# Optimization experiments

Hardware: AMD Instinct MI355X
Metric: run time of the kernel (lower is better)

## Reference

```python
import jax, jax.numpy as jnp
import numpy as np

DIM = 2048
N_HEADS = 16
N_KV_HEADS = 4
HEAD_DIM = DIM // N_HEADS  # 128
ROPE_BASE = 10000.0
QK_GAIN_INIT = 1.0
RMS_EPS = 1.1920928955078125e-07  # torch F.rms_norm default eps = finfo(fp32).eps


def _rms_norm(x):
    # normalize over last dim, no learned gain
    var = jnp.mean(jnp.square(x), axis=-1, keepdims=True)
    return x * jax.lax.rsqrt(var + RMS_EPS)


def _rope_cos_sin(seq_len, dtype):
    half = HEAD_DIM // 2
    inv_freq = 1.0 / (ROPE_BASE ** (jnp.arange(0, HEAD_DIM, 2, dtype=jnp.float32) / HEAD_DIM))
    t = jnp.arange(seq_len, dtype=jnp.float32)
    freqs = jnp.outer(t, inv_freq)  # [S, half]
    return jnp.cos(freqs).astype(dtype), jnp.sin(freqs).astype(dtype)


def _apply_rotary(x, cos, sin):
    # x: [B, H, S, D]; cos/sin: [S, D//2] broadcast over B,H
    half = x.shape[-1] // 2
    x1, x2 = x[..., :half], x[..., half:]
    return jnp.concatenate((x1 * cos + x2 * sin, x1 * (-sin) + x2 * cos), axis=-1)


def setup_inputs() -> dict:
    key = jax.random.key(0)
    ks = jax.random.split(key, 6)
    B, S = 2, 2048
    kv_dim = N_KV_HEADS * HEAD_DIM
    x = jax.random.normal(ks[0], (B, S, DIM), dtype=jnp.float32)
    Wq = jax.random.normal(ks[1], (DIM, DIM), dtype=jnp.float32) * (DIM ** -0.5)
    Wk = jax.random.normal(ks[2], (kv_dim, DIM), dtype=jnp.float32) * (DIM ** -0.5)
    Wv = jax.random.normal(ks[3], (kv_dim, DIM), dtype=jnp.float32) * (DIM ** -0.5)
    Wproj = jax.random.normal(ks[4], (DIM, DIM), dtype=jnp.float32) * (DIM ** -0.5)
    q_gain = jnp.full((N_HEADS,), QK_GAIN_INIT, dtype=jnp.float32)
    return {"x": x, "Wq": Wq, "Wk": Wk, "Wv": Wv, "Wproj": Wproj, "q_gain": q_gain}


def reference(x, Wq, Wk, Wv, Wproj, q_gain):
    B, S, D = x.shape
    G = N_HEADS // N_KV_HEADS  # GQA group size
    # QKV projections (CastedLinear, no bias)
    q = (x @ Wq.T).reshape(B, S, N_HEADS, HEAD_DIM).transpose(0, 2, 1, 3)      # [B,H,S,d]
    k = (x @ Wk.T).reshape(B, S, N_KV_HEADS, HEAD_DIM).transpose(0, 2, 1, 3)   # [B,Hkv,S,d]
    v = (x @ Wv.T).reshape(B, S, N_KV_HEADS, HEAD_DIM).transpose(0, 2, 1, 3)
    # QK RMS-norm
    q = _rms_norm(q)
    k = _rms_norm(k)
    # RoPE (scaling='none' -> attention_factor = 1.0)
    cos, sin = _rope_cos_sin(S, q.dtype)
    q = _apply_rotary(q, cos, sin)
    k = _apply_rotary(k, cos, sin)
    # per-head query gain * attention_factor (=1.0)
    q = q * q_gain.astype(q.dtype)[None, :, None, None]
    # causal GQA SDPA: group queries by kv head, no k/v materialized repeats
    qg = q.reshape(B, N_KV_HEADS, G, S, HEAD_DIM)
    scale = 1.0 / jnp.sqrt(jnp.asarray(HEAD_DIM, dtype=q.dtype))
    scores = jnp.einsum('bkgqd,bkld->bkgql', qg, k) * scale  # [B,Hkv,G,S,S]
    causal = jnp.tril(jnp.ones((S, S), dtype=bool))
    scores = jnp.where(causal, scores, jnp.asarray(-jnp.inf, dtype=scores.dtype))
    attn = jax.nn.softmax(scores, axis=-1)
    y = jnp.einsum('bkgql,bkld->bkgqd', attn, v)              # [B,Hkv,G,S,d]
    y = y.reshape(B, N_HEADS, S, HEAD_DIM).transpose(0, 2, 1, 3).reshape(B, S, D)
    return y @ Wproj.T
```

## Files before the change

### kernel.cpp

```cpp
#include <hip/hip_runtime.h>
#include <hip/hip_bf16.h>

#define DIM 2048
#define NH 16
#define NKV 4
#define HD 128
#define S_LEN 2048
#define BATCH 2
#define QKV_N 3072
#define NEGBIG -1.0e30f

typedef __attribute__((ext_vector_type(8))) short bf16x8;
typedef __attribute__((ext_vector_type(4))) float f32x4;
typedef unsigned short ushort_t;

#define GLOAD_LDS16(gp, lp)                                                       \
    __builtin_amdgcn_global_load_lds(                                             \
        (const __attribute__((address_space(1))) void*)(gp),                      \
        (__attribute__((address_space(3))) void*)(lp), 16, 0, 0)

static __device__ __forceinline__ ushort_t f2bf(float f) {
    union { float f; unsigned u; } v; v.f = f;
    unsigned r = v.u + 0x7fffu + ((v.u >> 16) & 1u);
    return (ushort_t)(r >> 16);
}
static __device__ __forceinline__ float bf2f(ushort_t u) {
    union { unsigned u; float f; } v; v.u = ((unsigned)u) << 16;
    return v.f;
}
static __device__ __forceinline__ unsigned pk2bf(float a, float b) {
    unsigned r;
    __asm__ volatile("v_cvt_pk_bf16_f32 %0, %1, %2" : "=v"(r) : "v"(a), "v"(b));
    return r;
}

__global__ __launch_bounds__(256) void cvt_in(const float* __restrict__ x,
                                              const float* __restrict__ Wq,
                                              const float* __restrict__ Wk,
                                              const float* __restrict__ Wv,
                                              const float* __restrict__ Wp,
                                              ushort_t* __restrict__ xb,
                                              ushort_t* __restrict__ Wqkvb,
                                              ushort_t* __restrict__ Wpb) {
    int i = (blockIdx.x * 256 + threadIdx.x) * 4;
    const float* src;
    ushort_t* dst;
    int soff, doff;
    if (i < 8388608) {
        src = x; dst = xb; soff = i; doff = i;
    } else if (i < 14680064) {
        int j = i - 8388608;
        dst = Wqkvb; doff = j;
        if (j < 4194304) { src = Wq; soff = j; }
        else if (j < 5242880) { src = Wk; soff = j - 4194304; }
        else { src = Wv; soff = j - 5242880; }
    } else {
        int j = i - 14680064;
        src = Wp; dst = Wpb; soff = j; doff = j;
    }
    float4 v = *(const float4*)&src[soff];
    uint2 o = {pk2bf(v.x, v.y), pk2bf(v.z, v.w)};
    *(uint2*)&dst[doff] = o;
}

#define FENCE() __asm__ __volatile__("" ::: "memory")
#define BARRIER() do { FENCE(); __builtin_amdgcn_s_barrier(); FENCE(); } while (0)
#define WAITVM(n) __asm__ __volatile__("s_waitcnt vmcnt(" #n ")" ::: "memory")
#define WLGKM0() __asm__ __volatile__("s_waitcnt lgkmcnt(0)" ::: "memory")

#define STG(LDSA, GP, rowb) do {                                                  \
    const int r_ = (rowb) + rsub;                                                 \
    GLOAD_LDS16(&(GP)[(size_t)r_ * 2048 + kk0_ + ((csw0 ^ (r_ & 7)) * 8)],        \
                &(LDSA)[(rowb) * 64]);                                            \
} while (0)

#define STAGE_HT(AB, BB, kt, ht) do {                                             \
    const int kt_ = (kt) < 31 ? (kt) : 31;                                        \
    const int kk0_ = kt_ * 64;                                                    \
    if ((ht) == 0)      { STG(BB, Bp, w8);       STG(BB, Bp, 64 + w8);  }         \
    else if ((ht) == 1) { STG(BB, Bp, 128 + w8); STG(BB, Bp, 192 + w8); }         \
    else if ((ht) == 2) { STG(AB, Ap, w8);       STG(AB, Ap, 128 + w8); }         \
    else                { STG(AB, Ap, 64 + w8);  STG(AB, Ap, 192 + w8); }         \
} while (0)

#define DSA(mtb, AS) do {                                                         \
    _Pragma("unroll") for (int dm = 0; dm < 2; dm++)                              \
    _Pragma("unroll") for (int ks = 0; ks < 2; ks++) {                            \
        const int row = wr * 128 + ((mtb) + dm) * 16 + m16;                       \
        af[dm][ks] = *(const bf16x8*)&(AS)[row * 64 +                             \
                                           (((ks * 4 + quad) ^ (row & 7)) * 8)];  \
    }                                                                             \
} while (0)

#define DSB(BS) do {                                                              \
    _Pragma("unroll") for (int nt = 0; nt < 4; nt++)                              \
    _Pragma("unroll") for (int ks = 0; ks < 2; ks++) {                            \
        const int row = wc * 64 + nt * 16 + m16;                                  \
        bfr[nt][ks] = *(const bf16x8*)&(BS)[row * 64 +                            \
                                            (((ks * 4 + quad) ^ (row & 7)) * 8)]; \
    }                                                                             \
} while (0)

#define MMA(mtb) do {                                                             \
    __builtin_amdgcn_s_setprio(1);                                                \
    _Pragma("unroll") for (int ks = 0; ks < 2; ks++)                              \
    _Pragma("unroll") for (int dm = 0; dm < 2; dm++)                              \
    _Pragma("unroll") for (int nt = 0; nt < 4; nt++)                              \
        acc[(mtb) + dm][nt] = __builtin_amdgcn_mfma_f32_16x16x32_bf16(            \
            af[dm][ks], bfr[nt][ks], acc[(mtb) + dm][nt], 0, 0, 0);               \
    __builtin_amdgcn_s_setprio(0);                                                \
} while (0)

template <int EPI>
__global__ __launch_bounds__(512, 2) void gemm256(const ushort_t* __restrict__ A,
                                                  const ushort_t* __restrict__ B,
                                                  float* __restrict__ C,
                                                  ushort_t* __restrict__ qkv,
                                                  ushort_t* __restrict__ vt,
                                                  const float* __restrict__ gain,
                                                  int N) {
    __shared__ __align__(16) ushort_t sh[4][256 * 64];
    const int t = threadIdx.x;
    const int lane = t & 63;
    const int wave = t >> 6;
    const int m16 = lane & 15;
    const int quad = lane >> 4;
    const int wr = wave >> 2;
    const int wc = wave & 3;
    const int nwg = gridDim.x * gridDim.y;
    const int wgid = blockIdx.y * gridDim.x + blockIdx.x;
    const int wg2 = (wgid & 7) * (nwg >> 3) + (wgid >> 3);
    const int bx = wg2 % gridDim.x;
    const int m0 = (wg2 / gridDim.x) * 256;
    const int n0 = bx * 256;
    const int rsub = lane >> 3;
    const int csw0 = lane & 7;
    const int w8 = wave * 8;
    const ushort_t* Ap = A + (size_t)m0 * 2048;
    const ushort_t* Bp = B + (size_t)n0 * 2048;

    f32x4 acc[8][4];
#pragma unroll
    for (int i = 0; i < 8; i++)
#pragma unroll
        for (int j = 0; j < 4; j++) acc[i][j] = (f32x4){0.f, 0.f, 0.f, 0.f};

    STAGE_HT(sh[0], sh[2], 0, 0);
    STAGE_HT(sh[0], sh[2], 0, 1);
    STAGE_HT(sh[0], sh[2], 0, 2);
    STAGE_HT(sh[0], sh[2], 0, 3);
    STAGE_HT(sh[1], sh[3], 1, 0);
    STAGE_HT(sh[1], sh[3], 1, 1);
    STAGE_HT(sh[1], sh[3], 1, 2);
    WAITVM(6);
    BARRIER();

    bf16x8 bfr[4][2];
#pragma unroll 1
    for (int i = 0; i < 16; ++i) {
        const int tb = 2 * i;
        {
            bf16x8 af[2][2];
            DSA(0, sh[0]); DSB(sh[2]);
            STAGE_HT(sh[1], sh[3], tb + 1, 3);
            WLGKM0(); MMA(0); BARRIER();
        }
        {
            bf16x8 af[2][2];
            DSA(2, sh[0]);
            STAGE_HT(sh[0], sh[2], tb + 2, 0);
            WLGKM0(); MMA(2); BARRIER();
        }
        {
            bf16x8 af[2][2];
            DSA(4, sh[0]);
            STAGE_HT(sh[0], sh[2], tb + 2, 1);
            WLGKM0(); MMA(4); BARRIER();
        }
        {
            bf16x8 af[2][2];
            DSA(6, sh[0]);
            STAGE_HT(sh[0], sh[2], tb + 2, 2);
            WAITVM(6);
            WLGKM0(); MMA(6); BARRIER();
        }
        {
            bf16x8 af[2][2];
            DSA(0, sh[1]); DSB(sh[3]);
            STAGE_HT(sh[0], sh[2], tb + 2, 3);
            WLGKM0(); MMA(0); BARRIER();
        }
        {
            bf16x8 af[2][2];
            DSA(2, sh[1]);
            STAGE_HT(sh[1], sh[3], tb + 3, 0);
            WLGKM0(); MMA(2); BARRIER();
        }
        {
            bf16x8 af[2][2];
            DSA(4, sh[1]);
            STAGE_HT(sh[1], sh[3], tb + 3, 1);
            WLGKM0(); MMA(4); BARRIER();
        }
        {
            bf16x8 af[2][2];
            DSA(6, sh[1]);
            STAGE_HT(sh[1], sh[3], tb + 3, 2);
            WAITVM(6);
            WLGKM0(); MMA(6); BARRIER();
        }
    }
    WAITVM(0);
    __syncthreads();

    if constexpr (EPI == 0) {
#pragma unroll
        for (int mt = 0; mt < 8; mt++)
#pragma unroll
            for (int r = 0; r < 4; r++) {
                const int row = m0 + wr * 128 + mt * 16 + quad * 4 + r;
#pragma unroll
                for (int nt = 0; nt < 4; nt++)
                    C[(size_t)row * N + n0 + wc * 64 + nt * 16 + m16] = acc[mt][nt][r];
            }
    } else {
        ushort_t* Cs = &sh[0][0];
#pragma unroll
        for (int mt = 0; mt < 8; mt++)
#pragma unroll
            for (int r = 0; r < 4; r++) {
                const int row = wr * 128 + mt * 16 + quad * 4 + r;
#pragma unroll
                for (int nt = 0; nt < 4; nt++)
                    Cs[row * 256 + wc * 64 + nt * 16 + m16] = f2bf(acc[mt][nt][r]);
            }
        __syncthreads();

        if (bx < 10) {
            const float invf = exp2f(-0.20762050593046f * (float)lane);
            float gg[2];
#pragma unroll
            for (int hh = 0; hh < 2; hh++) gg[hh] = (bx < 8) ? gain[bx * 2 + hh] : 1.0f;
#pragma unroll 2
            for (int i = 0; i < 32; i++) {
                const int row = wave * 32 + i;
                const int m = m0 + row;
                const int s = m & (S_LEN - 1);
                const float fr = (float)s * invf;
                const float c = cosf(fr), sn = sinf(fr);
#pragma unroll
                for (int hh = 0; hh < 2; hh++) {
                    float x1 = bf2f(Cs[row * 256 + hh * 128 + lane]);
                    float x2 = bf2f(Cs[row * 256 + hh * 128 + 64 + lane]);
                    float ss = x1 * x1 + x2 * x2;
#pragma unroll
                    for (int mm = 32; mm >= 1; mm >>= 1) ss += __shfl_xor(ss, mm, 64);
                    const float rms = rsqrtf(ss * (1.0f / 128.0f) + 1.1920928955078125e-07f);
                    x1 *= rms; x2 *= rms;
                    ushort_t* dst = qkv + (size_t)m * QKV_N + bx * 256 + hh * 128;
                    dst[lane] = f2bf((x1 * c + x2 * sn) * gg[hh]);
                    dst[lane + 64] = f2bf((x2 * c - x1 * sn) * gg[hh]);
                }
            }
        } else {
            const int half = t >> 8;
            const int tt = t & 255;
            const int d = tt >> 1;
            const int so = (tt & 1) * 128;
            const int b = m0 >> 11;
            const int s0 = m0 & (S_LEN - 1);
            const int kv = (bx - 10) * 2 + half;
            ushort_t* dst = vt + ((size_t)(b * NKV + kv) * HD + d) * S_LEN + s0 + so;
#pragma unroll
            for (int j0 = 0; j0 < 128; j0 += 8) {
                ushort_t tmp[8];
#pragma unroll
                for (int j = 0; j < 8; j++) tmp[j] = Cs[(so + j0 + j) * 256 + half * 128 + d];
                *(uint4*)&dst[j0] = *(uint4*)tmp;
            }
        }
    }
}

__device__ __constant__ short attn_tab[24][4] = {
    {15, 0, 16, 14}, {15, 16, 32, 15}, {7, 0, 16, -1}, {14, 0, 15, 12},
    {13, 0, 14, 10}, {13, 14, 28, 11}, {6, 0, 14, -1}, {10, 0, 11, 4},
    {12, 0, 13, 8},  {12, 13, 26, 9}, {14, 15, 30, 13}, {11, 0, 12, 6},
    {11, 12, 24, 7}, {5, 0, 12, -1}, {10, 11, 22, 5},  {9, 0, 10, 2},
    {2, 0, 6, -1},   {1, 0, 4, -1},  {0, 0, 2, -1},    {3, 0, 8, -1},
    {8, 0, 9, 0},    {8, 9, 18, 1},  {9, 10, 20, 3},   {4, 0, 10, -1},
};

__global__ __launch_bounds__(256) void attn(const ushort_t* __restrict__ QKV,
                                            const ushort_t* __restrict__ Vt,
                                            ushort_t* __restrict__ Y,
                                            ushort_t* __restrict__ Po,
                                            float* __restrict__ Pl) {
    __shared__ __align__(16) ushort_t Ks[64 * 128];
    __shared__ __align__(16) ushort_t Vs[128 * 64];
    __shared__ __align__(16) ushort_t Ps[4][32 * 72];
    const int lane = threadIdx.x & 63;
    const int wave = threadIdx.x >> 6;
    const int m16 = lane & 15, quad = lane >> 4;
    const int seg = blockIdx.x >> 5;
    const int hb = blockIdx.x & 31;
    const int h = hb & (NH - 1), b = hb >> 4;
    const int kvh = h >> 2;
    const int bx = attn_tab[seg][0];
    const int t0 = attn_tab[seg][1];
    const int t1 = attn_tab[seg][2];
    const int slotl = attn_tab[seg][3];
    const int q0w = bx * 128 + wave * 32;

    const ushort_t* kbase = QKV + (size_t)b * S_LEN * QKV_N + DIM + kvh * HD;
    const ushort_t* vbase = Vt + (size_t)(b * NKV + kvh) * (HD * S_LEN);

    bf16x8 bq[2][4];
#pragma unroll
    for (int g = 0; g < 2; g++)
#pragma unroll
        for (int ks = 0; ks < 4; ks++)
            bq[g][ks] = *(const bf16x8*)&QKV[((size_t)(b * S_LEN + q0w + g * 16 + m16)) * QKV_N +
                                             h * HD + ks * 32 + quad * 8];

    float ls[2] = {0.f, 0.f};
    f32x4 o[2][8];
#pragma unroll
    for (int g = 0; g < 2; g++)
#pragma unroll
        for (int nd = 0; nd < 8; nd++) o[g][nd] = (f32x4){0.f, 0.f, 0.f, 0.f};

    ushort_t* pw = Ps[wave];
    for (int t = t0; t < t1; ++t) {
        const int kv0 = t * 64;
        __syncthreads();
#pragma unroll
        for (int i = 0; i < 4; i++) {
            const int c0 = i * 256 + wave * 64;
            const int ck = c0 + lane;
            const int krow = ck >> 4;
            const int kcol = (ck & 15) ^ (krow & 7);
            GLOAD_LDS16(kbase + (size_t)(kv0 + krow) * QKV_N + kcol * 8, &Ks[c0 * 8]);
            const int vd = ck >> 3;
            const int vcol = (ck & 7) ^ (vd & 7);
            GLOAD_LDS16(vbase + (size_t)vd * S_LEN + kv0 + vcol * 8, &Vs[c0 * 8]);
        }
        __syncthreads();

        f32x4 st[2][4];
#pragma unroll
        for (int g = 0; g < 2; g++)
#pragma unroll
            for (int nt = 0; nt < 4; nt++) st[g][nt] = (f32x4){0.f, 0.f, 0.f, 0.f};
#pragma unroll
        for (int ks = 0; ks < 4; ks++)
#pragma unroll
            for (int nt = 0; nt < 4; nt++) {
                const int row = nt * 16 + m16;
                bf16x8 ak = *(const bf16x8*)&Ks[row * 128 + (((ks * 4 + quad) ^ (row & 7)) * 8)];
#pragma unroll
                for (int g = 0; g < 2; g++)
                    st[g][nt] = __builtin_amdgcn_mfma_f32_16x16x32_bf16(ak, bq[g][ks],
                                                                        st[g][nt], 0, 0, 0);
            }
#pragma unroll
        for (int g = 0; g < 2; g++) {
            const int q0g = q0w + g * 16;
            const int qg = q0g + m16;
            const bool interior = (kv0 + 63 <= q0g);
            float rs = 0.f;
#pragma unroll
            for (int nt = 0; nt < 4; nt++) {
                float p[4];
#pragma unroll
                for (int r = 0; r < 4; r++) {
                    float x = st[g][nt][r] * 0.08838834764831845f;
                    if (!interior) {
                        const int kg = kv0 + nt * 16 + quad * 4 + r;
                        x = (kg > qg) ? NEGBIG : x;
                    }
                    p[r] = __expf(x);
                }
                rs += (p[0] + p[1]) + (p[2] + p[3]);
                uint2 pk = {pk2bf(p[0], p[1]), pk2bf(p[2], p[3])};
                *(uint2*)&pw[(g * 16 + m16) * 72 + nt * 16 + quad * 4] = pk;
            }
            ls[g] += rs;
        }
        __asm__ __volatile__("s_waitcnt lgkmcnt(0)" ::: "memory");
        bf16x8 bp[2][2];
#pragma unroll
        for (int g = 0; g < 2; g++)
#pragma unroll
            for (int kk = 0; kk < 2; kk++)
                bp[g][kk] = *(const bf16x8*)&pw[(g * 16 + m16) * 72 + kk * 32 + quad * 8];
#pragma unroll
        for (int kk = 0; kk < 2; kk++)
#pragma unroll
            for (int nd = 0; nd < 8; nd++) {
                const int vrow = nd * 16 + m16;
                bf16x8 av = *(const bf16x8*)&Vs[vrow * 64 + (((kk * 4 + quad) ^ (vrow & 7)) * 8)];
#pragma unroll
                for (int g = 0; g < 2; g++)
                    o[g][nd] = __builtin_amdgcn_mfma_f32_16x16x32_bf16(av, bp[g][kk],
                                                                       o[g][nd], 0, 0, 0);
            }
    }
    float l_tot[2];
#pragma unroll
    for (int g = 0; g < 2; g++) {
        float v = ls[g];
        v += __shfl_xor(v, 16, 64);
        v += __shfl_xor(v, 32, 64);
        l_tot[g] = v;
    }
    if (slotl < 0) {
#pragma unroll
        for (int g = 0; g < 2; g++) {
            const float inv = 1.0f / l_tot[g];
            const int qg = q0w + g * 16 + m16;
            ushort_t* yp = Y + ((size_t)(b * S_LEN + qg)) * DIM + h * HD;
#pragma unroll
            for (int nd = 0; nd < 8; nd++) {
                uint2 pk = {pk2bf(o[g][nd][0] * inv, o[g][nd][1] * inv),
                            pk2bf(o[g][nd][2] * inv, o[g][nd][3] * inv)};
                *(uint2*)&yp[nd * 16 + quad * 4] = pk;
            }
        }
    } else if ((slotl & 1) == 0) {
        const int slot = ((b * NH + h) << 4) + slotl;
#pragma unroll
        for (int g = 0; g < 2; g++) {
            const int qg = q0w + g * 16 + m16;
            ushort_t* yp = Y + ((size_t)(b * S_LEN + qg)) * DIM + h * HD;
#pragma unroll
            for (int nd = 0; nd < 8; nd++) {
                uint2 pk = {pk2bf(o[g][nd][0], o[g][nd][1]),
                            pk2bf(o[g][nd][2], o[g][nd][3])};
                *(uint2*)&yp[nd * 16 + quad * 4] = pk;
            }
            if (quad == 0) Pl[slot * 128 + wave * 32 + g * 16 + m16] = l_tot[g];
        }
    } else {
        const int slot = ((b * NH + h) << 4) + slotl;
        ushort_t* po = Po + (size_t)(((b * NH + h) << 3) + (slotl >> 1)) * (128 * 128);
#pragma unroll
        for (int g = 0; g < 2; g++) {
            const int ql = wave * 32 + g * 16 + m16;
#pragma unroll
            for (int nd = 0; nd < 8; nd++) {
                uint2 pk = {pk2bf(o[g][nd][0], o[g][nd][1]),
                            pk2bf(o[g][nd][2], o[g][nd][3])};
                *(uint2*)&po[ql * 128 + nd * 16 + quad * 4] = pk;
            }
            if (quad == 0) Pl[slot * 128 + ql] = l_tot[g];
        }
    }
}

__global__ __launch_bounds__(256) void attn_combine(const ushort_t* __restrict__ Po,
                                                    const float* __restrict__ Pl,
                                                    ushort_t* __restrict__ Y) {
    const int R = blockIdx.x * 2 + (threadIdx.x >> 7);
    const int d = threadIdx.x & 127;
    const int q = R & 127;
    const int bx8 = (R >> 7) & 7;
    const int h = (R >> 10) & 15;
    const int b = R >> 14;
    const int hb16 = ((b * NH + h) << 4);
    const float l0 = Pl[(hb16 + bx8 * 2) * 128 + q];
    const float l1 = Pl[(hb16 + bx8 * 2 + 1) * 128 + q];
    const float inv = 1.0f / (l0 + l1);
    const int qg = (bx8 + 8) * 128 + q;
    ushort_t* yp = Y + ((size_t)(b * S_LEN + qg)) * DIM + h * HD + d;
    const float o0 = bf2f(*yp);
    const float o1 = bf2f(Po[(size_t)(((b * NH + h) << 3) + bx8) * (128 * 128) + q * 128 + d]);
    *yp = f2bf((o0 + o1) * inv);
}

extern "C" void kernel_launch(void* const* d_in, const int* in_sizes, int n_in,
                              void* d_out, int out_size, void* d_ws, size_t ws_size,
                              hipStream_t stream) {
    (void)in_sizes; (void)n_in; (void)out_size; (void)ws_size;
    const float* xf  = (const float*)d_in[0];
    const float* Wqf = (const float*)d_in[1];
    const float* Wkf = (const float*)d_in[2];
    const float* Wvf = (const float*)d_in[3];
    const float* Wpf = (const float*)d_in[4];
    const float* gn  = (const float*)d_in[5];
    float* out = (float*)d_out;

    char* ws = (char*)d_ws;
    ushort_t* xb    = (ushort_t*)(ws);
    ushort_t* qkv   = (ushort_t*)(ws + (16ull << 20));
    ushort_t* vt    = (ushort_t*)(ws + (40ull << 20));
    ushort_t* Wqkvb = (ushort_t*)(ws + (44ull << 20));
    ushort_t* Wpb   = (ushort_t*)(ws + (56ull << 20));
    ushort_t* y     = xb;
    ushort_t* Po    = (ushort_t*)(ws + (44ull << 20));
    float*    Pl    = (float*)(ws + (52ull << 20));

    const int M = BATCH * S_LEN;
    cvt_in<<<dim3(18432), 256, 0, stream>>>(xf, Wqf, Wkf, Wvf, Wpf, xb, Wqkvb, Wpb);
    gemm256<1><<<dim3(QKV_N / 256, M / 256), 512, 0, stream>>>(xb, Wqkvb, nullptr, qkv, vt, gn, 0);
    attn<<<dim3(768, 1, 1), 256, 0, stream>>>(qkv, vt, y, Po, Pl);
    attn_combine<<<dim3(BATCH * NH * 8 * 128 / 2), 256, 0, stream>>>(Po, Pl, y);
    gemm256<0><<<dim3(DIM / 256, M / 256), 512, 0, stream>>>(y, Wpb, out, nullptr, nullptr, nullptr, DIM);
}
```

Before: 305.9 us.

## Use dedicated 128x256-tile pipelined GEMM for output projection

Splits the templated GEMM into a QKV-specific kernel and a new output-projection kernel that uses 128x256 tiles with its own double-buffered LDS staging schedule. The smaller M tile doubles the grid for the 4096x2048x2048 projection from 128 to 256 workgroups, improving occupancy and wave balance across the CUs. The cost is lower arithmetic intensity per tile and more A/B reloads from L2.

```diff
diff --git a/kernel.cpp b/kernel.cpp
--- a/kernel.cpp
+++ b/kernel.cpp
@@ -111,14 +111,11 @@
     __builtin_amdgcn_s_setprio(0);                                                \
 } while (0)
 
-template <int EPI>
-__global__ __launch_bounds__(512, 2) void gemm256(const ushort_t* __restrict__ A,
-                                                  const ushort_t* __restrict__ B,
-                                                  float* __restrict__ C,
-                                                  ushort_t* __restrict__ qkv,
-                                                  ushort_t* __restrict__ vt,
-                                                  const float* __restrict__ gain,
-                                                  int N) {
+__global__ __launch_bounds__(512, 2) void gemm256_qkv(const ushort_t* __restrict__ A,
+                                                      const ushort_t* __restrict__ B,
+                                                      ushort_t* __restrict__ qkv,
+                                                      ushort_t* __restrict__ vt,
+                                                      const float* __restrict__ gain) {
     __shared__ __align__(16) ushort_t sh[4][256 * 64];
     const int t = threadIdx.x;
     const int lane = t & 63;
@@ -159,51 +156,43 @@
 #pragma unroll 1
     for (int i = 0; i < 16; ++i) {
         const int tb = 2 * i;
-        {
-            bf16x8 af[2][2];
+        {   bf16x8 af[2][2];
             DSA(0, sh[0]); DSB(sh[2]);
             STAGE_HT(sh[1], sh[3], tb + 1, 3);
             WLGKM0(); MMA(0); BARRIER();
         }
-        {
-            bf16x8 af[2][2];
+        {   bf16x8 af[2][2];
             DSA(2, sh[0]);
             STAGE_HT(sh[0], sh[2], tb + 2, 0);
             WLGKM0(); MMA(2); BARRIER();
         }
-        {
-            bf16x8 af[2][2];
+        {   bf16x8 af[2][2];
             DSA(4, sh[0]);
             STAGE_HT(sh[0], sh[2], tb + 2, 1);
             WLGKM0(); MMA(4); BARRIER();
         }
-        {
-            bf16x8 af[2][2];
+        {   bf16x8 af[2][2];
             DSA(6, sh[0]);
             STAGE_HT(sh[0], sh[2], tb + 2, 2);
             WAITVM(6);
             WLGKM0(); MMA(6); BARRIER();
         }
-        {
-            bf16x8 af[2][2];
+        {   bf16x8 af[2][2];
             DSA(0, sh[1]); DSB(sh[3]);
             STAGE_HT(sh[0], sh[2], tb + 2, 3);
             WLGKM0(); MMA(0); BARRIER();
         }
-        {
-            bf16x8 af[2][2];
+        {   bf16x8 af[2][2];
             DSA(2, sh[1]);
             STAGE_HT(sh[1], sh[3], tb + 3, 0);
             WLGKM0(); MMA(2); BARRIER();
         }
-        {
-            bf16x8 af[2][2];
+        {   bf16x8 af[2][2];
             DSA(4, sh[1]);
             STAGE_HT(sh[1], sh[3], tb + 3, 1);
             WLGKM0(); MMA(4); BARRIER();
         }
-        {
-            bf16x8 af[2][2];
+        {   bf16x8 af[2][2];
             DSA(6, sh[1]);
             STAGE_HT(sh[1], sh[3], tb + 3, 2);
             WAITVM(6);
@@ -213,73 +202,180 @@
     WAITVM(0);
     __syncthreads();
 
-    if constexpr (EPI == 0) {
-#pragma unroll
-        for (int mt = 0; mt < 8; mt++)
-#pragma unroll
-            for (int r = 0; r < 4; r++) {
-                const int row = m0 + wr * 128 + mt * 16 + quad * 4 + r;
-#pragma unroll
-                for (int nt = 0; nt < 4; nt++)
-                    C[(size_t)row * N + n0 + wc * 64 + nt * 16 + m16] = acc[mt][nt][r];
+    ushort_t* Cs = &sh[0][0];
+#pragma unroll
+    for (int mt = 0; mt < 8; mt++)
+#pragma unroll
+        for (int r = 0; r < 4; r++) {
+            const int row = wr * 128 + mt * 16 + quad * 4 + r;
+#pragma unroll
+            for (int nt = 0; nt < 4; nt++)
+                Cs[row * 256 + wc * 64 + nt * 16 + m16] = f2bf(acc[mt][nt][r]);
+        }
+    __syncthreads();
+
+    if (bx < 10) {
+        const float invf = exp2f(-0.20762050593046f * (float)lane);
+        float gg[2];
+#pragma unroll
+        for (int hh = 0; hh < 2; hh++) gg[hh] = (bx < 8) ? gain[bx * 2 + hh] : 1.0f;
+#pragma unroll 2
+        for (int i = 0; i < 32; i++) {
+            const int row = wave * 32 + i;
+            const int m = m0 + row;
+            const int s = m & (S_LEN - 1);
+            const float fr = (float)s * invf;
+            const float c = cosf(fr), sn = sinf(fr);
+#pragma unroll
+            for (int hh = 0; hh < 2; hh++) {
+                float x1 = bf2f(Cs[row * 256 + hh * 128 + lane]);
+                float x2 = bf2f(Cs[row * 256 + hh * 128 + 64 + lane]);
+                float ss = x1 * x1 + x2 * x2;
+#pragma unroll
+                for (int mm = 32; mm >= 1; mm >>= 1) ss += __shfl_xor(ss, mm, 64);
+                const float rms = rsqrtf(ss * (1.0f / 128.0f) + 1.1920928955078125e-07f);
+                x1 *= rms; x2 *= rms;
+                ushort_t* dst = qkv + (size_t)m * QKV_N + bx * 256 + hh * 128;
+                dst[lane] = f2bf((x1 * c + x2 * sn) * gg[hh]);
+                dst[lane + 64] = f2bf((x2 * c - x1 * sn) * gg[hh]);
             }
+        }
     } else {
-        ushort_t* Cs = &sh[0][0];
-#pragma unroll
-        for (int mt = 0; mt < 8; mt++)
-#pragma unroll
-            for (int r = 0; r < 4; r++) {
-                const int row = wr * 128 + mt * 16 + quad * 4 + r;
-#pragma unroll
-                for (int nt = 0; nt < 4; nt++)
-                    Cs[row * 256 + wc * 64 + nt * 16 + m16] = f2bf(acc[mt][nt][r]);
-            }
-        __syncthreads();
-
-        if (bx < 10) {
-            const float invf = exp2f(-0.20762050593046f * (float)lane);
-            float gg[2];
-#pragma unroll
-            for (int hh = 0; hh < 2; hh++) gg[hh] = (bx < 8) ? gain[bx * 2 + hh] : 1.0f;
-#pragma unroll 2
-            for (int i = 0; i < 32; i++) {
-                const int row = wave * 32 + i;
-                const int m = m0 + row;
-                const int s = m & (S_LEN - 1);
-                const float fr = (float)s * invf;
-                const float c = cosf(fr), sn = sinf(fr);
-#pragma unroll
-                for (int hh = 0; hh < 2; hh++) {
-                    float x1 = bf2f(Cs[row * 256 + hh * 128 + lane]);
-                    float x2 = bf2f(Cs[row * 256 + hh * 128 + 64 + lane]);
-                    float ss = x1 * x1 + x2 * x2;
-#pragma unroll
-                    for (int mm = 32; mm >= 1; mm >>= 1) ss += __shfl_xor(ss, mm, 64);
-                    const float rms = rsqrtf(ss * (1.0f / 128.0f) + 1.1920928955078125e-07f);
-                    x1 *= rms; x2 *= rms;
-                    ushort_t* dst = qkv + (size_t)m * QKV_N + bx * 256 + hh * 128;
-                    dst[lane] = f2bf((x1 * c + x2 * sn) * gg[hh]);
-                    dst[lane + 64] = f2bf((x2 * c - x1 * sn) * gg[hh]);
-                }
-            }
-        } else {
-            const int half = t >> 8;
-            const int tt = t & 255;
-            const int d = tt >> 1;
-            const int so = (tt & 1) * 128;
-            const int b = m0 >> 11;
-            const int s0 = m0 & (S_LEN - 1);
-            const int kv = (bx - 10) * 2 + half;
-            ushort_t* dst = vt + ((size_t)(b * NKV + kv) * HD + d) * S_LEN + s0 + so;
-#pragma unroll
-            for (int j0 = 0; j0 < 128; j0 += 8) {
-                ushort_t tmp[8];
-#pragma unroll
-                for (int j = 0; j < 8; j++) tmp[j] = Cs[(so + j0 + j) * 256 + half * 128 + d];
-                *(uint4*)&dst[j0] = *(uint4*)tmp;
-            }
+        const int half = t >> 8;
+        const int tt = t & 255;
+        const int d = tt >> 1;
+        const int so = (tt & 1) * 128;
+        const int b = m0 >> 11;
+        const int s0 = m0 & (S_LEN - 1);
+        const int kv = (bx - 10) * 2 + half;
+        ushort_t* dst = vt + ((size_t)(b * NKV + kv) * HD + d) * S_LEN + s0 + so;
+#pragma unroll
+        for (int j0 = 0; j0 < 128; j0 += 8) {
+            ushort_t tmp[8];
+#pragma unroll
+            for (int j = 0; j < 8; j++) tmp[j] = Cs[(so + j0 + j) * 256 + half * 128 + d];
+            *(uint4*)&dst[j0] = *(uint4*)tmp;
         }
     }
+}
+
+#define P_STAGE_A(AB, kt) do {                                                    \
+    const int kt_ = (kt) < 31 ? (kt) : 31;                                        \
+    const int kk0_ = kt_ * 64;                                                    \
+    STG(AB, Ap, w8); STG(AB, Ap, 64 + w8);                                        \
+} while (0)
+#define P_STAGE_BLO(BB, kt) do {                                                  \
+    const int kt_ = (kt) < 31 ? (kt) : 31;                                        \
+    const int kk0_ = kt_ * 64;                                                    \
+    STG(BB, Bp, w8); STG(BB, Bp, 64 + w8);                                        \
+} while (0)
+#define P_STAGE_BHI(BB, kt) do {                                                  \
+    const int kt_ = (kt) < 31 ? (kt) : 31;                                        \
+    const int kk0_ = kt_ * 64;                                                    \
+    STG(BB, Bp, 128 + w8); STG(BB, Bp, 192 + w8);                                 \
+} while (0)
+
+#define P_DSA8(AS) do {                                                           \
+    _Pragma("unroll") for (int mt = 0; mt < 4; mt++)                              \
+    _Pragma("unroll") for (int ks = 0; ks < 2; ks++) {                            \
+        const int row = wr * 64 + mt * 16 + m16;                                  \
+        af[mt][ks] = *(const bf16x8*)&(AS)[row * 64 +                             \
+                                           (((ks * 4 + quad) ^ (row & 7)) * 8)];  \
+    }                                                                             \
+} while (0)
+#define P_DSB(BS, base, arr) do {                                                 \
+    _Pragma("unroll") for (int nt = 0; nt < 2; nt++)                              \
+    _Pragma("unroll") for (int ks = 0; ks < 2; ks++) {                            \
+        const int row = wc * 64 + (base) + nt * 16 + m16;                         \
+        arr[nt][ks] = *(const bf16x8*)&(BS)[row * 64 +                            \
+                                            (((ks * 4 + quad) ^ (row & 7)) * 8)]; \
+    }                                                                             \
+} while (0)
+
+#define P_MMA(ntb, arr) do {                                                      \
+    __builtin_amdgcn_s_setprio(1);                                                \
+    _Pragma("unroll") for (int ks = 0; ks < 2; ks++)                              \
+    _Pragma("unroll") for (int mt = 0; mt < 4; mt++)                              \
+    _Pragma("unroll") for (int nt = 0; nt < 2; nt++)                              \
+        acc[mt][(ntb) + nt] = __builtin_amdgcn_mfma_f32_16x16x32_bf16(            \
+            af[mt][ks], arr[nt][ks], acc[mt][(ntb) + nt], 0, 0, 0);               \
+    __builtin_amdgcn_s_setprio(0);                                                \
+} while (0)
+
+__global__ __launch_bounds__(512, 2) void gemm_proj(const ushort_t* __restrict__ A,
+                                                    const ushort_t* __restrict__ B,
+                                                    float* __restrict__ C) {
+    __shared__ __align__(16) ushort_t Asb[2][128 * 64];
+    __shared__ __align__(16) ushort_t Bsb[2][256 * 64];
+    const int t = threadIdx.x;
+    const int lane = t & 63;
+    const int wave = t >> 6;
+    const int m16 = lane & 15;
+    const int quad = lane >> 4;
+    const int wr = wave >> 2;
+    const int wc = wave & 3;
+    const int nwg = gridDim.x * gridDim.y;
+    const int wgid = blockIdx.y * gridDim.x + blockIdx.x;
+    const int wg2 = (wgid & 7) * (nwg >> 3) + (wgid >> 3);
+    const int bx = wg2 % gridDim.x;
+    const int m0 = (wg2 / gridDim.x) * 128;
+    const int n0 = bx * 256;
+    const int rsub = lane >> 3;
+    const int csw0 = lane & 7;
+    const int w8 = wave * 8;
+    const ushort_t* Ap = A + (size_t)m0 * 2048;
+    const ushort_t* Bp = B + (size_t)n0 * 2048;
+
+    f32x4 acc[4][4];
+#pragma unroll
+    for (int i = 0; i < 4; i++)
+#pragma unroll
+        for (int j = 0; j < 4; j++) acc[i][j] = (f32x4){0.f, 0.f, 0.f, 0.f};
+
+    P_STAGE_A(Asb[0], 0); P_STAGE_BLO(Bsb[0], 0); P_STAGE_BHI(Bsb[0], 0);
+    P_STAGE_A(Asb[1], 1); P_STAGE_BLO(Bsb[1], 1);
+    WAITVM(4);
+    BARRIER();
+
+    bf16x8 af[4][2], bl[2][2], bh[2][2];
+#pragma unroll 1
+    for (int i = 0; i < 16; ++i) {
+        const int tb = 2 * i;
+        {
+            P_DSA8(Asb[0]); P_DSB(Bsb[0], 0, bl);
+            P_STAGE_BHI(Bsb[1], tb + 1);
+            WLGKM0(); P_MMA(0, bl); BARRIER();
+        }
+        {
+            P_DSB(Bsb[0], 32, bh);
+            P_STAGE_A(Asb[0], tb + 2); P_STAGE_BLO(Bsb[0], tb + 2);
+            WAITVM(4);
+            WLGKM0(); P_MMA(2, bh); BARRIER();
+        }
+        {
+            P_DSA8(Asb[1]); P_DSB(Bsb[1], 0, bl);
+            P_STAGE_BHI(Bsb[0], tb + 2);
+            WLGKM0(); P_MMA(0, bl); BARRIER();
+        }
+        {
+            P_DSB(Bsb[1], 32, bh);
+            P_STAGE_A(Asb[1], tb + 3); P_STAGE_BLO(Bsb[1], tb + 3);
+            WAITVM(4);
+            WLGKM0(); P_MMA(2, bh); BARRIER();
+        }
+    }
+    WAITVM(0);
+    __syncthreads();
+
+#pragma unroll
+    for (int mt = 0; mt < 4; mt++)
+#pragma unroll
+        for (int r = 0; r < 4; r++) {
+            const int row = m0 + wr * 64 + mt * 16 + quad * 4 + r;
+#pragma unroll
+            for (int nt = 0; nt < 4; nt++)
+                C[(size_t)row * DIM + n0 + wc * 64 + nt * 16 + m16] = acc[mt][nt][r];
+        }
 }
 
 __device__ __constant__ short attn_tab[24][4] = {
@@ -502,8 +598,8 @@
 
     const int M = BATCH * S_LEN;
     cvt_in<<<dim3(18432), 256, 0, stream>>>(xf, Wqf, Wkf, Wvf, Wpf, xb, Wqkvb, Wpb);
-    gemm256<1><<<dim3(QKV_N / 256, M / 256), 512, 0, stream>>>(xb, Wqkvb, nullptr, qkv, vt, gn, 0);
+    gemm256_qkv<<<dim3(QKV_N / 256, M / 256), 512, 0, stream>>>(xb, Wqkvb, qkv, vt, gn);
     attn<<<dim3(768, 1, 1), 256, 0, stream>>>(qkv, vt, y, Po, Pl);
     attn_combine<<<dim3(BATCH * NH * 8 * 128 / 2), 256, 0, stream>>>(Po, Pl, y);
-    gemm256<0><<<dim3(DIM / 256, M / 256), 512, 0, stream>>>(y, Wpb, out, nullptr, nullptr, nullptr, DIM);
-}
+    gemm_proj<<<dim3(DIM / 256, M / 128), 512, 0, stream>>>(y, Wpb, out);
+}
```

After: 292.5 us. -4.4%, faster.
